# Performance work log

Hardware: AMD Instinct MI355X
Metric: run time of the kernel (lower is better)

## Reference

```python
import jax, jax.numpy as jnp
import numpy as np

HEADS = 16
D_Q = 64
D_K = 64
D_V = 64
MODEL_DIM = 1024
LN_EPS = 1e-5


def setup_inputs() -> dict:
    key = jax.random.key(0)
    ks = jax.random.split(key, 6)
    B, S = 64, 4096
    data_input = jax.random.normal(ks[0], (B, S, MODEL_DIM), dtype=jnp.float32)
    # nn.Parameter(torch.randn(...)) -> unit normal weights
    weight_q = jax.random.normal(ks[1], (MODEL_DIM, HEADS * D_Q), dtype=jnp.float32)
    weight_k = jax.random.normal(ks[2], (MODEL_DIM, HEADS * D_K), dtype=jnp.float32)
    weight_v = jax.random.normal(ks[3], (MODEL_DIM, HEADS * D_V), dtype=jnp.float32)
    # nn.Linear(heads*d_v, model_dim): weight (out,in), uniform(-1/sqrt(in), 1/sqrt(in))
    bound = 1.0 / np.sqrt(HEADS * D_V)
    fc_weight = jax.random.uniform(ks[4], (MODEL_DIM, HEADS * D_V), minval=-bound, maxval=bound, dtype=jnp.float32)
    fc_bias = jax.random.uniform(ks[5], (MODEL_DIM,), minval=-bound, maxval=bound, dtype=jnp.float32)
    ln_gamma = jnp.ones((MODEL_DIM,), dtype=jnp.float32)
    ln_beta = jnp.zeros((MODEL_DIM,), dtype=jnp.float32)
    return {
        "data_input": data_input,
        "weight_q": weight_q,
        "weight_k": weight_k,
        "weight_v": weight_v,
        "fc_weight": fc_weight,
        "fc_bias": fc_bias,
        "ln_gamma": ln_gamma,
        "ln_beta": ln_beta,
        "index": 4095,
    }


def reference(data_input, weight_q, weight_k, weight_v, fc_weight, fc_bias, ln_gamma, ln_beta, index):
    # data_input: (B, S_max, D); causal single-query attention at position `index`
    involved = data_input[:, : index + 1, :]            # (B, S, D)
    B, S, _ = involved.shape
    q = involved @ weight_q                              # (B, S, H*dq)
    k = involved @ weight_k                              # (B, S, H*dk)
    v = involved @ weight_v                              # (B, S, H*dv)
    target_q = q[:, -1:, :]                              # (B, 1, H*dq) query at `index`
    # per-head dot-product scores: sum over d of target_q*k, per head
    scores = jnp.sum(
        target_q.reshape(B, 1, HEADS, D_Q) * k.reshape(B, S, HEADS, D_K), axis=-1
    ) / jnp.sqrt(jnp.float32(D_K))                       # (B, S, H)
    attn = jax.nn.softmax(scores, axis=1)                # softmax over sequence
    # weighted sum of values per head -> concat heads
    head_out = jnp.sum(v.reshape(B, S, HEADS, D_V) * attn[..., None], axis=1)  # (B, H, dv)
    concat = head_out.reshape(B, 1, HEADS * D_V)         # (B, 1, H*dv)
    integrated = concat @ fc_weight.T + fc_bias          # (B, 1, D)
    mean = jnp.mean(integrated, axis=-1, keepdims=True)
    var = jnp.mean(jnp.square(integrated - mean), axis=-1, keepdims=True)
    normed = (integrated - mean) * jax.lax.rsqrt(var + LN_EPS)
    return normed * ln_gamma + ln_beta
```

## Files before the change

### kernel.cpp

```cpp
#include <hip/hip_runtime.h>
#include <math.h>

#define B_   64
#define MD   1024
#define H_   16
#define D_   64
#define LNEPS 1e-5f


__device__ __forceinline__ float waveMax(float v) {
    #pragma unroll
    for (int off = 32; off > 0; off >>= 1) v = fmaxf(v, __shfl_xor(v, off, 64));
    return v;
}
__device__ __forceinline__ float waveSum(float v) {
    #pragma unroll
    for (int off = 32; off > 0; off >>= 1) v += __shfl_xor(v, off, 64);
    return v;
}

__global__ void k_q(const float* __restrict__ x, const float* __restrict__ wq,
                    const int* __restrict__ idxp, float* __restrict__ qout, int sfull) {
    const int tid = threadIdx.x;
    const int col = blockIdx.x * 256 + tid;
    const int b   = blockIdx.y;
    const int idx = *idxp;
    const float* xr = x + ((size_t)b * sfull + idx) * MD;
    float a0 = 0.f, a1 = 0.f, a2 = 0.f, a3 = 0.f;
    for (int m = 0; m < MD; m += 4) {
        a0 += xr[m]     * wq[(size_t)m * MD + col];
        a1 += xr[m + 1] * wq[(size_t)(m + 1) * MD + col];
        a2 += xr[m + 2] * wq[(size_t)(m + 2) * MD + col];
        a3 += xr[m + 3] * wq[(size_t)(m + 3) * MD + col];
    }
    qout[(size_t)b * MD + col] = (a0 + a1) + (a2 + a3);
}

__global__ void k_wtil(const float* __restrict__ wk, const float* __restrict__ q,
                       float* __restrict__ wtil) {
    const int tid = threadIdx.x;
    const int h  = blockIdx.x;
    const int b0 = blockIdx.y * 2;
    for (int mi = 0; mi < 4; ++mi) {
        const int m = mi * 256 + tid;
        const float4* wrow = (const float4*)(wk + (size_t)m * MD + h * D_);
        float4 wv[16];
        #pragma unroll
        for (int j = 0; j < 16; ++j) wv[j] = wrow[j];
        #pragma unroll
        for (int bb = 0; bb < 2; ++bb) {
            const float* qh = q + (size_t)(b0 + bb) * MD + h * D_;
            float acc = 0.f;
            #pragma unroll
            for (int j = 0; j < 16; ++j)
                acc += wv[j].x * qh[4*j] + wv[j].y * qh[4*j+1]
                     + wv[j].z * qh[4*j+2] + wv[j].w * qh[4*j+3];
            wtil[((size_t)(b0 + bb) * H_ + h) * MD + m] = acc;
        }
    }
}

__global__ __launch_bounds__(256) void k_scores(
        const float* __restrict__ x, const float* __restrict__ wtil,
        const int* __restrict__ idxp, float* __restrict__ scores, int sfull) {
    __shared__ float Xw[4][128 * 20];
    __shared__ float Ww[4][16 * 20];
    const int tid  = threadIdx.x;
    const int w    = tid >> 6;
    const int lane = tid & 63;
    const int sg   = lane & 15;
    const int hg   = lane >> 4;
    const int b    = blockIdx.x;
    const int sblk = blockIdx.y * 512;
    const int s0   = sblk + w * 128;
    const int S    = *idxp + 1;
    if (sblk >= S) return;

    const float* xb = x    + (size_t)b * sfull * MD;
    const float* wb = wtil + (size_t)b * H_ * MD;

    float* Xs = Xw[w];
    float* Ws = Ww[w];

    const int csl = lane >> 2;
    const int cf4 = lane & 3;

    const int phase = (b + blockIdx.y * 8 + w) & 63;
#define MCOF(T) ((((T) + phase) & 63) * 16)

    float acc[8][4] = {};
    float4 nx[8];
    float4 nw;

#define ISSUE(MC) do {                                                         \
        _Pragma("unroll")                                                      \
        for (int i = 0; i < 8; ++i) {                                          \
            int sl = i * 16 + csl;                                             \
            int srow = s0 + sl;                                                \
            nx[i] = (srow < S)                                                 \
                ? *(const float4*)(xb + (size_t)srow * MD + (MC) + cf4 * 4)    \
                : make_float4(0.f, 0.f, 0.f, 0.f);                             \
        }                                                                      \
        nw = *(const float4*)(wb + (size_t)csl * MD + (MC) + cf4 * 4);         \
    } while (0)

    ISSUE(MCOF(0));

    for (int t = 0; t < 64; ++t) {
        #pragma unroll
        for (int i = 0; i < 8; ++i)
            *(float4*)(&Xs[(i * 16 + csl) * 20 + cf4 * 4]) = nx[i];
        *(float4*)(&Ws[csl * 20 + cf4 * 4]) = nw;

        if (t + 1 < 64) ISSUE(MCOF(t + 1));

        #pragma unroll
        for (int half = 0; half < 2; ++half) {
            float4 wrh[4][2];
            #pragma unroll
            for (int j = 0; j < 4; ++j) {
                #pragma unroll
                for (int mm = 0; mm < 2; ++mm)
                    wrh[j][mm] = *(const float4*)(&Ws[(hg + 4 * j) * 20 + (half * 2 + mm) * 4]);
            }
            #pragma unroll
            for (int k = 0; k < 8; ++k) {
                const float4 xr0 = *(const float4*)(&Xs[(sg + 16 * k) * 20 + (half * 2) * 4]);
                const float4 xr1 = *(const float4*)(&Xs[(sg + 16 * k) * 20 + (half * 2 + 1) * 4]);
                #pragma unroll
                for (int j = 0; j < 4; ++j) {
                    acc[k][j] += xr0.x * wrh[j][0].x + xr0.y * wrh[j][0].y
                               + xr0.z * wrh[j][0].z + xr0.w * wrh[j][0].w
                               + xr1.x * wrh[j][1].x + xr1.y * wrh[j][1].y
                               + xr1.z * wrh[j][1].z + xr1.w * wrh[j][1].w;
                }
            }
        }
    }
#undef ISSUE
#undef MCOF

    #pragma unroll
    for (int k = 0; k < 8; ++k) {
        const int s = s0 + sg + 16 * k;
        if (s < S) {
            #pragma unroll
            for (int j = 0; j < 4; ++j)
                scores[((size_t)b * H_ + (hg + 4 * j)) * sfull + s] = acc[k][j] * 0.125f;
        }
    }
}

__global__ void k_attn(const float* __restrict__ x, const float* __restrict__ scores,
                       const float* __restrict__ wv, const int* __restrict__ idxp,
                       float* __restrict__ concat, int sfull) {
    __shared__ float red[8];
    __shared__ int   scanw[4];
    __shared__ int   lidx[4096];
    __shared__ float lw[4096];
    __shared__ float ylds[1024];
    __shared__ float pred[256];

    const int tid = threadIdx.x;
    const int h = blockIdx.x, b = blockIdx.y;
    const int S = *idxp + 1;
    const float* sc = scores + ((size_t)b * H_ + h) * sfull;

    float ls[16];
    float mx = -INFINITY;
    #pragma unroll
    for (int k = 0; k < 16; ++k) {
        int s = tid + 256 * k;
        if (s < S) { ls[k] = sc[s]; mx = fmaxf(mx, ls[k]); }
        else ls[k] = -INFINITY;
    }
    mx = waveMax(mx);
    const int wid = tid >> 6, lane = tid & 63;
    if (lane == 0) red[wid] = mx;
    __syncthreads();
    mx = fmaxf(fmaxf(red[0], red[1]), fmaxf(red[2], red[3]));

    float sum = 0.f; int cnt = 0;
    #pragma unroll
    for (int k = 0; k < 16; ++k) {
        if (ls[k] > -INFINITY) {
            float e = ls[k] - mx;
            sum += expf(e);
            if (e > -34.f) ++cnt;
        }
    }
    sum = waveSum(sum);
    __syncthreads();
    if (lane == 0) red[4 + wid] = sum;
    __syncthreads();
    const float inv = 1.f / (red[4] + red[5] + red[6] + red[7]);

    int inc = cnt;
    #pragma unroll
    for (int off = 1; off < 64; off <<= 1) {
        int t = __shfl_up(inc, off, 64);
        if (lane >= off) inc += t;
    }
    if (lane == 63) scanw[wid] = inc;
    __syncthreads();
    int wbase = 0, total = 0;
    #pragma unroll
    for (int ww = 0; ww < 4; ++ww) {
        int t = scanw[ww];
        if (ww < wid) wbase += t;
        total += t;
    }
    int pos = wbase + inc - cnt;
    #pragma unroll
    for (int k = 0; k < 16; ++k) {
        if (ls[k] > -INFINITY) {
            float e = ls[k] - mx;
            if (e > -34.f) { lidx[pos] = tid + 256 * k; lw[pos] = expf(e) * inv; ++pos; }
        }
    }
    __syncthreads();

    float4 acc = make_float4(0.f, 0.f, 0.f, 0.f);
    const float* xb = x + (size_t)b * sfull * MD;
    for (int e = 0; e < total; ++e) {
        int s = lidx[e]; float w = lw[e];
        float4 xv = *(const float4*)(xb + (size_t)s * MD + tid * 4);
        acc.x += w * xv.x; acc.y += w * xv.y; acc.z += w * xv.z; acc.w += w * xv.w;
    }
    *(float4*)(&ylds[tid * 4]) = acc;
    __syncthreads();

    const int d = tid & 63, g = tid >> 6;
    const float* wcol = wv + (size_t)h * D_ + d;
    float part = 0.f;
    for (int m = g * 256; m < g * 256 + 256; ++m)
        part += ylds[m] * wcol[(size_t)m * MD];
    pred[tid] = part;
    __syncthreads();
    if (tid < 64) {
        float v = pred[tid] + pred[tid + 64] + pred[tid + 128] + pred[tid + 192];
        concat[(size_t)b * MD + h * D_ + tid] = v;
    }
}

__global__ void k_transpose(const float* __restrict__ a, float* __restrict__ at) {
    __shared__ float t[32][33];
    const int bx = blockIdx.x * 32, by = blockIdx.y * 32;
    const int tx = threadIdx.x & 31, ty = threadIdx.x >> 5;
    for (int r = ty; r < 32; r += 8)
        t[r][tx] = a[(size_t)(by + r) * MD + bx + tx];
    __syncthreads();
    for (int r = ty; r < 32; r += 8)
        at[(size_t)(bx + r) * MD + by + tx] = t[tx][r];
}

__global__ void k_fc(const float* __restrict__ concat, const float* __restrict__ fcwt,
                     const float* __restrict__ bias, float* __restrict__ integ) {
    __shared__ float c[1024];
    __shared__ float pred[256];
    const int tid = threadIdx.x, b = blockIdx.x;
    const int n0 = blockIdx.y * 64;
    const int nl = tid & 63, mg = tid >> 6;
    #pragma unroll
    for (int k = 0; k < 4; ++k) c[tid + 256 * k] = concat[(size_t)b * MD + tid + 256 * k];
    __syncthreads();
    const int mbase = mg * 256;
    float a0 = 0.f, a1 = 0.f, a2 = 0.f, a3 = 0.f;
    for (int m = 0; m < 256; m += 4) {
        a0 += c[mbase + m]     * fcwt[(size_t)(mbase + m) * MD + n0 + nl];
        a1 += c[mbase + m + 1] * fcwt[(size_t)(mbase + m + 1) * MD + n0 + nl];
        a2 += c[mbase + m + 2] * fcwt[(size_t)(mbase + m + 2) * MD + n0 + nl];
        a3 += c[mbase + m + 3] * fcwt[(size_t)(mbase + m + 3) * MD + n0 + nl];
    }
    pred[tid] = (a0 + a1) + (a2 + a3);
    __syncthreads();
    if (tid < 64)
        integ[(size_t)b * MD + n0 + tid] =
            pred[tid] + pred[tid + 64] + pred[tid + 128] + pred[tid + 192] + bias[n0 + tid];
}

__global__ void k_ln(const float* __restrict__ integ, const float* __restrict__ gamma,
                     const float* __restrict__ beta, float* __restrict__ out) {
    __shared__ float red[8];
    const int tid = threadIdx.x, b = blockIdx.x;
    float v[4];
    #pragma unroll
    for (int k = 0; k < 4; ++k) v[k] = integ[(size_t)b * MD + tid + 256 * k];
    float s = v[0] + v[1] + v[2] + v[3];
    s = waveSum(s);
    const int wid = tid >> 6, lane = tid & 63;
    if (lane == 0) red[wid] = s;
    __syncthreads();
    const float mean = (red[0] + red[1] + red[2] + red[3]) * (1.f / MD);
    float q = 0.f;
    #pragma unroll
    for (int k = 0; k < 4; ++k) { float d = v[k] - mean; q += d * d; }
    q = waveSum(q);
    __syncthreads();
    if (lane == 0) red[4 + wid] = q;
    __syncthreads();
    const float var = (red[4] + red[5] + red[6] + red[7]) * (1.f / MD);
    const float rs = rsqrtf(var + LNEPS);
    #pragma unroll
    for (int k = 0; k < 4; ++k) {
        int i = tid + 256 * k;
        out[(size_t)b * MD + i] = (v[k] - mean) * rs * gamma[i] + beta[i];
    }
}

extern "C" void kernel_launch(void* const* d_in, const int* in_sizes, int n_in,
                              void* d_out, int out_size, void* d_ws, size_t ws_size,
                              hipStream_t stream) {
    const float* x     = (const float*)d_in[0];
    const float* wq    = (const float*)d_in[1];
    const float* wk    = (const float*)d_in[2];
    const float* wvp   = (const float*)d_in[3];
    const float* fcw   = (const float*)d_in[4];
    const float* fcb   = (const float*)d_in[5];
    const float* gamma = (const float*)d_in[6];
    const float* beta  = (const float*)d_in[7];
    const int*   idxp  = (const int*)d_in[8];
    float* out = (float*)d_out;

    const int sfull = in_sizes[0] / (B_ * MD);

    float* q      = (float*)d_ws;
    float* wtil   = q      + (size_t)B_ * MD;
    float* scores = wtil   + (size_t)B_ * H_ * MD;
    float* concat = scores + (size_t)B_ * H_ * sfull;
    float* integ  = concat + (size_t)B_ * MD;
    float* fcwt   = integ  + (size_t)B_ * MD;

    hipLaunchKernelGGL(k_q,         dim3(4, 64),           dim3(256), 0, stream, x, wq, idxp, q, sfull);
    hipLaunchKernelGGL(k_wtil,      dim3(16, 32),          dim3(256), 0, stream, wk, q, wtil);
    hipLaunchKernelGGL(k_scores,    dim3(B_, (sfull + 511) / 512), dim3(256), 0, stream, x, wtil, idxp, scores, sfull);
    hipLaunchKernelGGL(k_transpose, dim3(32, 32),          dim3(256), 0, stream, fcw, fcwt);
    hipLaunchKernelGGL(k_attn,      dim3(H_, B_),          dim3(256), 0, stream, x, scores, wvp, idxp, concat, sfull);
    hipLaunchKernelGGL(k_fc,        dim3(64, 16),          dim3(256), 0, stream, concat, fcwt, fcb, integ);
    hipLaunchKernelGGL(k_ln,        dim3(B_),              dim3(256), 0, stream, integ, gamma, beta, out);
}
```

Baseline: 349.4 us.

## Use split-bf16 MFMA for score computation in k_scores

```diff
diff --git a/kernel.cpp b/kernel.cpp
--- a/kernel.cpp
+++ b/kernel.cpp
@@ -7,6 +7,19 @@
 #define D_   64
 #define LNEPS 1e-5f
 
+
+typedef __attribute__((ext_vector_type(8))) short short8;
+typedef __attribute__((ext_vector_type(8))) unsigned short ushort8_t;
+typedef __attribute__((ext_vector_type(4))) float f32x4;
+
+__device__ __forceinline__ unsigned short f2bf(float f) {
+    unsigned int u = __float_as_uint(f);
+    u += 0x7fffu + ((u >> 16) & 1u);
+    return (unsigned short)(u >> 16);
+}
+__device__ __forceinline__ float bf2f(unsigned short h) {
+    return __uint_as_float(((unsigned int)h) << 16);
+}
 
 __device__ __forceinline__ float waveMax(float v) {
     #pragma unroll
@@ -63,90 +76,124 @@
 __global__ __launch_bounds__(256) void k_scores(
         const float* __restrict__ x, const float* __restrict__ wtil,
         const int* __restrict__ idxp, float* __restrict__ scores, int sfull) {
-    __shared__ float Xw[4][128 * 20];
-    __shared__ float Ww[4][16 * 20];
-    const int tid  = threadIdx.x;
-    const int w    = tid >> 6;
-    const int lane = tid & 63;
-    const int sg   = lane & 15;
-    const int hg   = lane >> 4;
-    const int b    = blockIdx.x;
-    const int sblk = blockIdx.y * 512;
-    const int s0   = sblk + w * 128;
-    const int S    = *idxp + 1;
+    __shared__ __align__(16) unsigned short Xh[4][128 * 32];
+    __shared__ __align__(16) unsigned short Xl[4][128 * 32];
+    __shared__ __align__(16) unsigned short Wh[4][16 * 32];
+    __shared__ __align__(16) unsigned short Wl[4][16 * 32];
+
+    const int tid   = threadIdx.x;
+    const int w     = tid >> 6;
+    const int lane  = tid & 63;
+    const int hquad = lane >> 4;
+    const int hs    = lane & 15;
+    const int b     = blockIdx.x;
+    const int sblk  = blockIdx.y * 512;
+    const int s0    = sblk + w * 128;
+    const int S     = *idxp + 1;
     if (sblk >= S) return;
 
     const float* xb = x    + (size_t)b * sfull * MD;
     const float* wb = wtil + (size_t)b * H_ * MD;
 
-    float* Xs = Xw[w];
-    float* Ws = Ww[w];
+    unsigned short* XhW = Xh[w];
+    unsigned short* XlW = Xl[w];
+    unsigned short* WhW = Wh[w];
+    unsigned short* WlW = Wl[w];
 
     const int csl = lane >> 2;
     const int cf4 = lane & 3;
-
-    const int phase = (b + blockIdx.y * 8 + w) & 63;
-#define MCOF(T) ((((T) + phase) & 63) * 16)
-
-    float acc[8][4] = {};
-    float4 nx[8];
-    float4 nw;
+    const int swk = (csl >> 1) & 3;
+    const int gW  = (cf4 ^ swk) * 8;
+
+    const int phase = (b + blockIdx.y * 8 + w) & 31;
+#define MCOF(T) ((((T) + phase) & 31) * 32)
+
+    f32x4 acc[8];
+    #pragma unroll
+    for (int T = 0; T < 8; ++T) { acc[T][0]=0.f; acc[T][1]=0.f; acc[T][2]=0.f; acc[T][3]=0.f; }
+
+    float4 nx[16];
+    float4 nw0, nw1;
 
 #define ISSUE(MC) do {                                                         \
         _Pragma("unroll")                                                      \
         for (int i = 0; i < 8; ++i) {                                          \
-            int sl = i * 16 + csl;                                             \
-            int srow = s0 + sl;                                                \
-            nx[i] = (srow < S)                                                 \
-                ? *(const float4*)(xb + (size_t)srow * MD + (MC) + cf4 * 4)    \
-                : make_float4(0.f, 0.f, 0.f, 0.f);                             \
+            int srow = s0 + i * 16 + csl;                                      \
+            if (srow < S) {                                                    \
+                nx[2*i]   = *(const float4*)(xb + (size_t)srow * MD + (MC) + cf4 * 8);     \
+                nx[2*i+1] = *(const float4*)(xb + (size_t)srow * MD + (MC) + cf4 * 8 + 4); \
+            } else {                                                           \
+                nx[2*i]   = make_float4(0.f, 0.f, 0.f, 0.f);                   \
+                nx[2*i+1] = make_float4(0.f, 0.f, 0.f, 0.f);                   \
+            }                                                                  \
         }                                                                      \
-        nw = *(const float4*)(wb + (size_t)csl * MD + (MC) + cf4 * 4);         \
+        nw0 = *(const float4*)(wb + (size_t)csl * MD + (MC) + cf4 * 8);        \
+        nw1 = *(const float4*)(wb + (size_t)csl * MD + (MC) + cf4 * 8 + 4);    \
     } while (0)
 
+#define CVT8(A, B, HV, LV) do {                                                \
+        (HV)[0]=f2bf((A).x); (LV)[0]=f2bf((A).x - bf2f((HV)[0]));              \
+        (HV)[1]=f2bf((A).y); (LV)[1]=f2bf((A).y - bf2f((HV)[1]));              \
+        (HV)[2]=f2bf((A).z); (LV)[2]=f2bf((A).z - bf2f((HV)[2]));              \
+        (HV)[3]=f2bf((A).w); (LV)[3]=f2bf((A).w - bf2f((HV)[3]));              \
+        (HV)[4]=f2bf((B).x); (LV)[4]=f2bf((B).x - bf2f((HV)[4]));              \
+        (HV)[5]=f2bf((B).y); (LV)[5]=f2bf((B).y - bf2f((HV)[5]));              \
+        (HV)[6]=f2bf((B).z); (LV)[6]=f2bf((B).z - bf2f((HV)[6]));              \
+        (HV)[7]=f2bf((B).w); (LV)[7]=f2bf((B).w - bf2f((HV)[7]));              \
+    } while (0)
+
+#define COMMIT() do {                                                          \
+        _Pragma("unroll")                                                      \
+        for (int i = 0; i < 8; ++i) {                                          \
+            ushort8_t hv, lv;                                                  \
+            CVT8(nx[2*i], nx[2*i+1], hv, lv);                                  \
+            const int off = (i * 16 + csl) * 32 + gW;                          \
+            *(ushort8_t*)(&XhW[off]) = hv;                                     \
+            *(ushort8_t*)(&XlW[off]) = lv;                                     \
+        }                                                                      \
+        {                                                                      \
+            ushort8_t hv, lv;                                                  \
+            CVT8(nw0, nw1, hv, lv);                                            \
+            const int off = csl * 32 + gW;                                     \
+            *(ushort8_t*)(&WhW[off]) = hv;                                     \
+            *(ushort8_t*)(&WlW[off]) = lv;                                     \
+        }                                                                      \
+    } while (0)
+
+    const int rkey  = (hs >> 1) & 3;
+    const int wgoff = hs * 32 + ((hquad ^ rkey) * 8);
+
     ISSUE(MCOF(0));
 
-    for (int t = 0; t < 64; ++t) {
+    for (int t = 0; t < 32; ++t) {
+        COMMIT();
+        if (t + 1 < 32) ISSUE(MCOF(t + 1));
+        short8 wfh = *(const short8*)(&WhW[wgoff]);
+        short8 wfl = *(const short8*)(&WlW[wgoff]);
         #pragma unroll
-        for (int i = 0; i < 8; ++i)
-            *(float4*)(&Xs[(i * 16 + csl) * 20 + cf4 * 4]) = nx[i];
-        *(float4*)(&Ws[csl * 20 + cf4 * 4]) = nw;
-
-        if (t + 1 < 64) ISSUE(MCOF(t + 1));
-
-        #pragma unroll
-        for (int half = 0; half < 2; ++half) {
-            float4 wrh[4][2];
-            #pragma unroll
-            for (int j = 0; j < 4; ++j) {
-                #pragma unroll
-                for (int mm = 0; mm < 2; ++mm)
-                    wrh[j][mm] = *(const float4*)(&Ws[(hg + 4 * j) * 20 + (half * 2 + mm) * 4]);
-            }
-            #pragma unroll
-            for (int k = 0; k < 8; ++k) {
-                const float4 xr0 = *(const float4*)(&Xs[(sg + 16 * k) * 20 + (half * 2) * 4]);
-                const float4 xr1 = *(const float4*)(&Xs[(sg + 16 * k) * 20 + (half * 2 + 1) * 4]);
-                #pragma unroll
-                for (int j = 0; j < 4; ++j) {
-                    acc[k][j] += xr0.x * wrh[j][0].x + xr0.y * wrh[j][0].y
-                               + xr0.z * wrh[j][0].z + xr0.w * wrh[j][0].w
-                               + xr1.x * wrh[j][1].x + xr1.y * wrh[j][1].y
-                               + xr1.z * wrh[j][1].z + xr1.w * wrh[j][1].w;
-                }
-            }
+        for (int T = 0; T < 8; ++T) {
+            const int xoff = (T * 16 + hs) * 32 + ((hquad ^ rkey) * 8);
+            short8 xfh = *(const short8*)(&XhW[xoff]);
+            acc[T] = __builtin_amdgcn_mfma_f32_16x16x32_bf16(wfh, xfh, acc[T], 0, 0, 0);
+            acc[T] = __builtin_amdgcn_mfma_f32_16x16x32_bf16(wfl, xfh, acc[T], 0, 0, 0);
+            short8 xfl = *(const short8*)(&XlW[xoff]);
+            acc[T] = __builtin_amdgcn_mfma_f32_16x16x32_bf16(wfh, xfl, acc[T], 0, 0, 0);
         }
     }
 #undef ISSUE
+#undef COMMIT
+#undef CVT8
 #undef MCOF
 
     #pragma unroll
-    for (int k = 0; k < 8; ++k) {
-        const int s = s0 + sg + 16 * k;
+    for (int T = 0; T < 8; ++T) {
+        const int s = s0 + T * 16 + hs;
         if (s < S) {
             #pragma unroll
-            for (int j = 0; j < 4; ++j)
-                scores[((size_t)b * H_ + (hg + 4 * j)) * sfull + s] = acc[k][j] * 0.125f;
+            for (int r = 0; r < 4; ++r) {
+                const int h = hquad * 4 + r;
+                scores[((size_t)b * H_ + h) * sfull + s] = acc[T][r] * 0.125f;
+            }
         }
     }
 }
```

Result: faster. 305.1 us (-12.7%).
